# Performance work log

Measured on AMD Instinct MI355X. Metric: run time of the kernel, lower is better.

The kernel has to match this reference:

```python
import jax, jax.numpy as jnp
import numpy as np

EPS = 1e-5  # torch LayerNorm default


def _layer_norm(x, w, b):
    # normalized_shape = [C, K, K] -> normalize over last 3 dims
    m = jnp.mean(x, axis=(-3, -2, -1), keepdims=True)
    v = jnp.var(x, axis=(-3, -2, -1), keepdims=True)
    return (x - m) * jax.lax.rsqrt(v + EPS) * w + b


def setup_inputs() -> dict:
    key = jax.random.key(0)
    k0, k1, k2, k3, k4, k5 = jax.random.split(key, 6)
    B, C, H, W, K = 32, 192, 56, 56, 7
    x = jax.random.normal(k0, (B, C, H, W), jnp.float32)
    ln0_w = jax.random.normal(k1, (C, K, K), jnp.float32)
    ln0_b = jax.random.normal(k2, (C, K, K), jnp.float32)
    conv0_w = jax.random.normal(k3, (C, 1, K, K), jnp.float32) * 0.1
    ln1_w = jax.random.normal(k4, (C, K, K), jnp.float32)
    ln1_b = jax.random.normal(k5, (C, K, K), jnp.float32)
    return {"x": x, "ln0_w": ln0_w, "ln0_b": ln0_b, "conv0_w": conv0_w,
            "ln1_w": ln1_w, "ln1_b": ln1_b}


def reference(x, ln0_w, ln0_b, conv0_w, ln1_w, ln1_b):
    B, C, H, W = x.shape
    K = conv0_w.shape[-1]
    # AdaptiveAvgPool2d((K,K)); H,W divisible by K -> uniform average pooling
    p = x.reshape(B, C, K, H // K, K, W // K).mean(axis=(3, 5))  # [B,C,K,K]
    p = _layer_norm(p, ln0_w, ln0_b)
    # depthwise KxK conv on KxK map, padding 'same'
    p = jax.lax.conv_general_dilated(
        p, conv0_w, window_strides=(1, 1), padding='SAME',
        dimension_numbers=('NCHW', 'OIHW', 'NCHW'), feature_group_count=C)
    p = jax.nn.relu(_layer_norm(p, ln1_w, ln1_b))  # [B,C,K,K] dynamic kernels
    # per-sample, per-channel depthwise conv: fold batch into channels
    ker = p.reshape(B * C, 1, K, K)
    out = jax.lax.conv_general_dilated(
        x.reshape(1, B * C, H, W), ker, window_strides=(1, 1), padding='SAME',
        dimension_numbers=('NCHW', 'OIHW', 'NCHW'), feature_group_count=B * C)
    return out.reshape(B, C, H, W)
```

## Files before the change

### kernel.cpp

```cpp
#include <hip/hip_runtime.h>

#define BB 32
#define CC 192
#define HH 56
#define WW 56
#define KS 7
#define HW 3136
#define KK 49
#define CKK 9408
#define PL 8
#define NCELL (BB * CC * KK)
#define NBC (BB * CC)
#define P0BLK 37
#define MIDBLK 24

typedef float f2 __attribute__((ext_vector_type(2)));

__global__ __launch_bounds__(256) void pool_kernel(const float* __restrict__ x,
                                                   float* __restrict__ p0,
                                                   float2* __restrict__ part0) {
    __shared__ float red[8];
    int b = blockIdx.x / P0BLK;
    int t = blockIdx.x - b * P0BLK;
    int cell = t * 256 + threadIdx.x;
    float v = 0.f;
    if (cell < CKK) {
        int c = cell / KK;
        int r = cell - c * KK;
        int i = r / KS;
        int j = r - i * KS;
        const float* src = x + ((size_t)(b * CC + c)) * HW + (i * PL) * WW + j * PL;
        float s = 0.f;
#pragma unroll
        for (int a = 0; a < PL; ++a) {
            float4 v0 = *(const float4*)(src + a * WW);
            float4 v1 = *(const float4*)(src + a * WW + 4);
            s += v0.x + v0.y + v0.z + v0.w + v1.x + v1.y + v1.z + v1.w;
        }
        v = s * (1.f / 64.f);
        p0[b * CKK + cell] = v;
    }
    float sv = v, sq = v * v;
#pragma unroll
    for (int o = 32; o > 0; o >>= 1) {
        sv += __shfl_down(sv, o, 64);
        sq += __shfl_down(sq, o, 64);
    }
    if ((threadIdx.x & 63) == 0) {
        red[(threadIdx.x >> 6) * 2 + 0] = sv;
        red[(threadIdx.x >> 6) * 2 + 1] = sq;
    }
    __syncthreads();
    if (threadIdx.x == 0)
        part0[blockIdx.x] = make_float2(red[0] + red[2] + red[4] + red[6],
                                        red[1] + red[3] + red[5] + red[7]);
}

__global__ __launch_bounds__(512) void mid_kernel(
    const float* __restrict__ p0,
    const float* __restrict__ ln0w, const float* __restrict__ ln0b,
    const float* __restrict__ w0,
    const float2* __restrict__ part0,
    float* __restrict__ q1,
    float2* __restrict__ part1)
{
    __shared__ float red[16];
    int tid  = threadIdx.x;
    int lane = tid & 63;
    int bc   = blockIdx.x * 8 + (tid >> 6);
    int b = bc / CC;
    int c = bc - b * CC;

    float s0 = 0.f, ss0 = 0.f;
    if (lane < P0BLK) {
        float2 p = part0[b * P0BLK + lane];
        s0 = p.x; ss0 = p.y;
    }
#pragma unroll
    for (int o = 32; o > 0; o >>= 1) {
        s0  += __shfl_down(s0, o, 64);
        ss0 += __shfl_down(ss0, o, 64);
    }
    s0  = __shfl(s0, 0, 64);
    ss0 = __shfl(ss0, 0, 64);
    float mean = s0 * (1.f / CKK);
    float rstd = rsqrtf(ss0 * (1.f / CKK) - mean * mean + 1e-5f);

    float val = 0.f;
    if (lane < KK)
        val = (p0[bc * KK + lane] - mean) * rstd * ln0w[c * KK + lane]
              + ln0b[c * KK + lane];

    int i0 = lane / KS;
    int j0 = lane - i0 * KS;
    const float* wc = w0 + c * KK;

    float acc = 0.f;
#pragma unroll
    for (int u = 0; u < KS; ++u) {
        int ii = i0 + u - 3;
#pragma unroll
        for (int v = 0; v < KS; ++v) {
            int jj = j0 + v - 3;
            bool ok = (ii >= 0) && (ii < KS) && (jj >= 0) && (jj < KS);
            int sl = ok ? (ii * KS + jj) : 0;
            float sv = __shfl(val, sl, 64);
            acc += ok ? sv * wc[u * KS + v] : 0.f;
        }
    }
    if (lane >= KK) acc = 0.f;
    if (lane < KK) q1[bc * KK + lane] = acc;

    float s2 = acc, ss2 = acc * acc;
#pragma unroll
    for (int o = 32; o > 0; o >>= 1) {
        s2  += __shfl_down(s2, o, 64);
        ss2 += __shfl_down(ss2, o, 64);
    }
    if (lane == 0) {
        red[(tid >> 6) * 2 + 0] = s2;
        red[(tid >> 6) * 2 + 1] = ss2;
    }
    __syncthreads();
    if (tid == 0) {
        float a = 0.f, q = 0.f;
#pragma unroll
        for (int w = 0; w < 8; ++w) { a += red[2 * w]; q += red[2 * w + 1]; }
        part1[blockIdx.x] = make_float2(a, q);
    }
}

#define TW2 64

__device__ __forceinline__ float rfl(float v) {
    return __int_as_float(__builtin_amdgcn_readfirstlane(__float_as_int(v)));
}

__device__ __forceinline__ void pkfma_dl(f2& acc, f2 vp, f2 tp) {
    asm("v_pk_fma_f32 %0, %1, %2, %0 op_sel_hi:[1,0,1]"
        : "+v"(acc) : "v"(vp), "s"(tp));
}
__device__ __forceinline__ void pkfma_dh(f2& acc, f2 vp, f2 tp) {
    asm("v_pk_fma_f32 %0, %1, %2, %0 op_sel:[0,1,0] op_sel_hi:[1,1,1]"
        : "+v"(acc) : "v"(vp), "s"(tp));
}
__device__ __forceinline__ void pkfma_x(f2& acc, f2 vp, f2 tp) {
    asm("v_pk_fma_f32 %0, %1, %2, %0 op_sel:[1,0,0] op_sel_hi:[0,1,1]"
        : "+v"(acc) : "v"(vp), "s"(tp));
}

__global__ __launch_bounds__(256) void conv_kernel(
    const float* __restrict__ x,
    const float* __restrict__ q1, const float2* __restrict__ part1,
    const float* __restrict__ ln1w, const float* __restrict__ ln1b,
    float* __restrict__ out)
{
    __shared__ f2 tile2[32 * TW2];
    __shared__ float kt[KK];
    __shared__ f2 dtab[16];
    __shared__ f2 ctab[28];
    int bc   = blockIdx.x;
    int b    = bc / CC;
    int c    = bc - b * CC;
    int tid  = threadIdx.x;
    int lane = tid & 63;
    int wid  = tid >> 6;

    float s1 = 0.f, ss1 = 0.f;
    if (lane < MIDBLK) {
        float2 p = part1[b * MIDBLK + lane];
        s1 = p.x; ss1 = p.y;
    }
#pragma unroll
    for (int o = 32; o > 0; o >>= 1) {
        s1  += __shfl_down(s1, o, 64);
        ss1 += __shfl_down(ss1, o, 64);
    }
    s1  = __shfl(s1, 0, 64);
    ss1 = __shfl(ss1, 0, 64);

    if (tid < KK) {
        float m = s1 * (1.f / CKK);
        float r = rsqrtf(ss1 * (1.f / CKK) - m * m + 1e-5f);
        float v = (q1[(size_t)bc * KK + tid] - m) * r * ln1w[c * KK + tid]
                  + ln1b[c * KK + tid];
        kt[tid] = v > 0.f ? v : 0.f;
    }

    for (int i = tid; i < 32 * TW2 / 2; i += 256)
        ((float4*)tile2)[i] = make_float4(0.f, 0.f, 0.f, 0.f);
    __syncthreads();

    if (tid < 28) {
        int d = tid / KS, v = tid - KS * d;
        f2 p;
        p.x = (d < 3) ? kt[(2 * d + 1) * KS + v] : 0.f;
        p.y = (d > 0) ? kt[(2 * d - 1) * KS + v] : 0.f;
        ctab[tid] = p;
    } else if (tid < 44) {
        int t = tid - 28;
        int d = t / 4, j = t - 4 * d;
        f2 p;
        p.x = kt[2 * d * KS + 2 * j];
        p.y = (2 * j + 1 < KS) ? kt[2 * d * KS + 2 * j + 1] : 0.f;
        dtab[t] = p;
    }

    const float* src = x + (size_t)bc * HW;
    for (int i = tid; i < 29 * 14; i += 256) {
        int pr2 = 1 + i / 14;
        int q   = i - (pr2 - 1) * 14;
        int rA  = 2 * pr2 - 3;
        int rB  = rA + 1;
        float4 a4 = (rA >= 0) ? *(const float4*)(src + rA * WW + 4 * q)
                              : make_float4(0.f, 0.f, 0.f, 0.f);
        float4 b4 = (rB < HH) ? *(const float4*)(src + rB * WW + 4 * q)
                              : make_float4(0.f, 0.f, 0.f, 0.f);
        f2* cell = tile2 + pr2 * TW2 + 3 + 4 * q;
        cell[0] = (f2){a4.x, b4.x};
        cell[1] = (f2){a4.y, b4.y};
        cell[2] = (f2){a4.z, b4.z};
        cell[3] = (f2){a4.w, b4.w};
    }
    __syncthreads();

    f2 dp[16], cp[28];
#pragma unroll
    for (int i = 0; i < 8; ++i) {
        float4 t4 = ((const float4*)dtab)[i];
        dp[2 * i]     = (f2){rfl(t4.x), rfl(t4.y)};
        dp[2 * i + 1] = (f2){rfl(t4.z), rfl(t4.w)};
    }
#pragma unroll
    for (int i = 0; i < 14; ++i) {
        float4 t4 = ((const float4*)ctab)[i];
        cp[2 * i]     = (f2){rfl(t4.x), rfl(t4.y)};
        cp[2 * i + 1] = (f2){rfl(t4.z), rfl(t4.w)};
    }

    int r0 = wid * 14;
    int R2 = wid * 7;
    f2 acc2[7];
#pragma unroll
    for (int t = 0; t < 7; ++t) acc2[t] = (f2){0.f, 0.f};

#pragma unroll
    for (int s = 0; s < 10; ++s) {
        const f2* cellp = tile2 + (R2 + s) * TW2 + lane;
        f2 v2[KS];
#pragma unroll
        for (int j = 0; j < KS; ++j) v2[j] = cellp[j];
#pragma unroll
        for (int d = 0; d < 4; ++d) {
            int t = s - d;
            if (t < 0 || t > 6) continue;
#pragma unroll
            for (int v = 0; v < KS; ++v) {
                if (v & 1) pkfma_dh(acc2[t], v2[v], dp[d * 4 + (v >> 1)]);
                else       pkfma_dl(acc2[t], v2[v], dp[d * 4 + (v >> 1)]);
                pkfma_x(acc2[t], v2[v], cp[d * KS + v]);
            }
        }
    }

    if (lane < WW) {
        float* ob = out + (size_t)bc * HW + r0 * WW + lane;
#pragma unroll
        for (int t = 0; t < 7; ++t) {
            ob[(2 * t) * WW]     = acc2[t].x;
            ob[(2 * t + 1) * WW] = acc2[t].y;
        }
    }
}

extern "C" void kernel_launch(void* const* d_in, const int* in_sizes, int n_in,
                              void* d_out, int out_size, void* d_ws, size_t ws_size,
                              hipStream_t stream) {
    const float* x    = (const float*)d_in[0];
    const float* ln0w = (const float*)d_in[1];
    const float* ln0b = (const float*)d_in[2];
    const float* w0   = (const float*)d_in[3];
    const float* ln1w = (const float*)d_in[4];
    const float* ln1b = (const float*)d_in[5];
    float* out = (float*)d_out;

    float*  p0    = (float*)d_ws;
    float*  q1    = p0 + NCELL;
    float2* part0 = (float2*)(q1 + NCELL);
    float2* part1 = part0 + BB * P0BLK;

    pool_kernel<<<BB * P0BLK, 256, 0, stream>>>(x, p0, part0);
    mid_kernel <<<BB * MIDBLK, 512, 0, stream>>>(p0, ln0w, ln0b, w0, part0, q1, part1);
    conv_kernel<<<NBC, 256, 0, stream>>>(x, q1, part1, ln1w, ln1b, out);
}
```

Measured before the change: 67.56 us.

## Compute two adjacent output columns per thread in conv kernel with 128 threads

The depthwise conv kernel drops from 256 to 128 threads per block. Each lane now computes two neighbouring output columns across 14 rows, sharing eight loaded input values, and reads LDS as float4 and writes output as float2. This halves the wavefront count and cuts LDS loads per FMA. The cost is more accumulator registers per thread and less thread-level parallelism per block.

Result: slower. 71.70 us (+6.1%).

```diff
diff --git a/kernel.cpp b/kernel.cpp
--- a/kernel.cpp
+++ b/kernel.cpp
@@ -149,7 +149,7 @@
         : "+v"(acc) : "v"(vp), "s"(tp));
 }
 
-__global__ __launch_bounds__(256) void conv_kernel(
+__global__ __launch_bounds__(128) void conv_kernel(
     const float* __restrict__ x,
     const float* __restrict__ q1, const float2* __restrict__ part1,
     const float* __restrict__ ln1w, const float* __restrict__ ln1b,
@@ -187,7 +187,7 @@
         kt[tid] = v > 0.f ? v : 0.f;
     }
 
-    for (int i = tid; i < 32 * TW2 / 2; i += 256)
+    for (int i = tid; i < 32 * TW2 / 2; i += 128)
         ((float4*)tile2)[i] = make_float4(0.f, 0.f, 0.f, 0.f);
     __syncthreads();
 
@@ -207,7 +207,7 @@
     }
 
     const float* src = x + (size_t)bc * HW;
-    for (int i = tid; i < 29 * 14; i += 256) {
+    for (int i = tid; i < 29 * 14; i += 128) {
         int pr2 = 1 + i / 14;
         int q   = i - (pr2 - 1) * 14;
         int rA  = 2 * pr2 - 3;
@@ -224,7 +224,7 @@
     }
     __syncthreads();
 
-    f2 dp[16], cp[28];
+    f2 dp[16], cpx[28];
 #pragma unroll
     for (int i = 0; i < 8; ++i) {
         float4 t4 = ((const float4*)dtab)[i];
@@ -234,41 +234,57 @@
 #pragma unroll
     for (int i = 0; i < 14; ++i) {
         float4 t4 = ((const float4*)ctab)[i];
-        cp[2 * i]     = (f2){rfl(t4.x), rfl(t4.y)};
-        cp[2 * i + 1] = (f2){rfl(t4.z), rfl(t4.w)};
-    }
-
-    int r0 = wid * 14;
-    int R2 = wid * 7;
-    f2 acc2[7];
-#pragma unroll
-    for (int t = 0; t < 7; ++t) acc2[t] = (f2){0.f, 0.f};
+        cpx[2 * i]     = (f2){rfl(t4.x), rfl(t4.y)};
+        cpx[2 * i + 1] = (f2){rfl(t4.z), rfl(t4.w)};
+    }
+
+    int rh = lane / 28;  if (rh > 1) rh = 1;
+    int cp = lane - 28 * (lane / 28); if (cp > 27) cp = 27;
+    int R2 = wid * 14 + rh * 7;
+
+    f2 accA[7], accB[7];
+#pragma unroll
+    for (int t = 0; t < 7; ++t) { accA[t] = (f2){0.f, 0.f}; accB[t] = (f2){0.f, 0.f}; }
 
 #pragma unroll
     for (int s = 0; s < 10; ++s) {
-        const f2* cellp = tile2 + (R2 + s) * TW2 + lane;
-        f2 v2[KS];
-#pragma unroll
-        for (int j = 0; j < KS; ++j) v2[j] = cellp[j];
+        const float4* rp = (const float4*)(tile2 + (R2 + s) * TW2 + 2 * cp);
+        float4 q0 = rp[0], q1v = rp[1], q2 = rp[2], q3 = rp[3];
+        f2 v2[8];
+        v2[0] = (f2){q0.x, q0.y}; v2[1] = (f2){q0.z, q0.w};
+        v2[2] = (f2){q1v.x, q1v.y}; v2[3] = (f2){q1v.z, q1v.w};
+        v2[4] = (f2){q2.x, q2.y}; v2[5] = (f2){q2.z, q2.w};
+        v2[6] = (f2){q3.x, q3.y}; v2[7] = (f2){q3.z, q3.w};
 #pragma unroll
         for (int d = 0; d < 4; ++d) {
             int t = s - d;
             if (t < 0 || t > 6) continue;
 #pragma unroll
-            for (int v = 0; v < KS; ++v) {
-                if (v & 1) pkfma_dh(acc2[t], v2[v], dp[d * 4 + (v >> 1)]);
-                else       pkfma_dl(acc2[t], v2[v], dp[d * 4 + (v >> 1)]);
-                pkfma_x(acc2[t], v2[v], cp[d * KS + v]);
+            for (int j = 0; j < 7; ++j) {
+                if (j & 1) pkfma_dh(accA[t], v2[j], dp[d * 4 + (j >> 1)]);
+                else       pkfma_dl(accA[t], v2[j], dp[d * 4 + (j >> 1)]);
+                pkfma_x(accA[t], v2[j], cpx[d * KS + j]);
+            }
+#pragma unroll
+            for (int j = 1; j < 8; ++j) {
+                int v = j - 1;
+                if (v & 1) pkfma_dh(accB[t], v2[j], dp[d * 4 + (v >> 1)]);
+                else       pkfma_dl(accB[t], v2[j], dp[d * 4 + (v >> 1)]);
+                pkfma_x(accB[t], v2[j], cpx[d * KS + v]);
             }
         }
     }
 
-    if (lane < WW) {
-        float* ob = out + (size_t)bc * HW + r0 * WW + lane;
+    if (lane < 56) {
+        float* ob = out + (size_t)bc * HW;
+        int col = 2 * cp;
+        int rowbase = wid * 28 + rh * 14;
 #pragma unroll
         for (int t = 0; t < 7; ++t) {
-            ob[(2 * t) * WW]     = acc2[t].x;
-            ob[(2 * t + 1) * WW] = acc2[t].y;
+            *(float2*)(ob + (rowbase + 2 * t) * WW + col) =
+                make_float2(accA[t].x, accB[t].x);
+            *(float2*)(ob + (rowbase + 2 * t + 1) * WW + col) =
+                make_float2(accA[t].y, accB[t].y);
         }
     }
 }
@@ -291,5 +307,5 @@
 
     pool_kernel<<<BB * P0BLK, 256, 0, stream>>>(x, p0, part0);
     mid_kernel <<<BB * MIDBLK, 512, 0, stream>>>(p0, ln0w, ln0b, w0, part0, q1, part1);
-    conv_kernel<<<NBC, 256, 0, stream>>>(x, q1, part1, ln1w, ln1b, out);
-}
+    conv_kernel<<<NBC, 128, 0, stream>>>(x, q1, part1, ln1w, ln1b, out);
+}
```

## Precompute dynamic kernel tables in separate kernel and prefetch input before barrier

Applied to the files above, without the earlier changes.

Moves the LayerNorm1/ReLU and packed coefficient-table construction out of the conv kernel into a new tab_kernel, one wave per (b,c), built with shuffles instead of shared memory. The conv kernel then loads the 44 packed coefficients straight from global memory. It also issues the input row loads into registers before the tile-zeroing barrier, so the load latency overlaps the zeroing. This removes a barrier and the per-block LN work from the conv kernel, at the cost of an extra kernel launch and a small workspace round trip. The coefficients are now loaded as uniform values without readfirstlane, so the compiler may have to prove uniformity to keep them in SGPRs.

Result: slower. 69.54 us (+2.9%).

```diff
diff --git a/kernel.cpp b/kernel.cpp
--- a/kernel.cpp
+++ b/kernel.cpp
@@ -130,41 +130,15 @@
     }
 }
 
-#define TW2 64
-
-__device__ __forceinline__ float rfl(float v) {
-    return __int_as_float(__builtin_amdgcn_readfirstlane(__float_as_int(v)));
-}
-
-__device__ __forceinline__ void pkfma_dl(f2& acc, f2 vp, f2 tp) {
-    asm("v_pk_fma_f32 %0, %1, %2, %0 op_sel_hi:[1,0,1]"
-        : "+v"(acc) : "v"(vp), "s"(tp));
-}
-__device__ __forceinline__ void pkfma_dh(f2& acc, f2 vp, f2 tp) {
-    asm("v_pk_fma_f32 %0, %1, %2, %0 op_sel:[0,1,0] op_sel_hi:[1,1,1]"
-        : "+v"(acc) : "v"(vp), "s"(tp));
-}
-__device__ __forceinline__ void pkfma_x(f2& acc, f2 vp, f2 tp) {
-    asm("v_pk_fma_f32 %0, %1, %2, %0 op_sel:[1,0,0] op_sel_hi:[0,1,1]"
-        : "+v"(acc) : "v"(vp), "s"(tp));
-}
-
-__global__ __launch_bounds__(256) void conv_kernel(
-    const float* __restrict__ x,
+__global__ __launch_bounds__(256) void tab_kernel(
     const float* __restrict__ q1, const float2* __restrict__ part1,
     const float* __restrict__ ln1w, const float* __restrict__ ln1b,
-    float* __restrict__ out)
+    f2* __restrict__ tab)
 {
-    __shared__ f2 tile2[32 * TW2];
-    __shared__ float kt[KK];
-    __shared__ f2 dtab[16];
-    __shared__ f2 ctab[28];
-    int bc   = blockIdx.x;
-    int b    = bc / CC;
-    int c    = bc - b * CC;
-    int tid  = threadIdx.x;
-    int lane = tid & 63;
-    int wid  = tid >> 6;
+    int lane = threadIdx.x & 63;
+    int bc   = blockIdx.x * 4 + (threadIdx.x >> 6);
+    int b = bc / CC;
+    int c = bc - b * CC;
 
     float s1 = 0.f, ss1 = 0.f;
     if (lane < MIDBLK) {
@@ -178,65 +152,114 @@
     }
     s1  = __shfl(s1, 0, 64);
     ss1 = __shfl(ss1, 0, 64);
-
-    if (tid < KK) {
-        float m = s1 * (1.f / CKK);
-        float r = rsqrtf(ss1 * (1.f / CKK) - m * m + 1e-5f);
-        float v = (q1[(size_t)bc * KK + tid] - m) * r * ln1w[c * KK + tid]
-                  + ln1b[c * KK + tid];
-        kt[tid] = v > 0.f ? v : 0.f;
+    float m = s1 * (1.f / CKK);
+    float r = rsqrtf(ss1 * (1.f / CKK) - m * m + 1e-5f);
+
+    float kt = 0.f;
+    if (lane < KK) {
+        float v = (q1[(size_t)bc * KK + lane] - m) * r * ln1w[c * KK + lane]
+                  + ln1b[c * KK + lane];
+        kt = v > 0.f ? v : 0.f;
+    }
+
+    int iA = 0, iB = 0;
+    bool mA = false, mB = false;
+    if (lane < 28) {
+        int d = lane / KS, v = lane - KS * d;
+        mA = (d < 3); iA = mA ? (2 * d + 1) * KS + v : 0;
+        mB = (d > 0); iB = mB ? (2 * d - 1) * KS + v : 0;
+    } else if (lane < 44) {
+        int t = lane - 28;
+        int d = t >> 2, j = t & 3;
+        mA = true;     iA = 2 * d * KS + 2 * j;
+        mB = (j < 3);  iB = mB ? 2 * d * KS + 2 * j + 1 : 0;
+    }
+    float va = __shfl(kt, iA, 64);
+    float vb = __shfl(kt, iB, 64);
+    f2 p;
+    p.x = mA ? va : 0.f;
+    p.y = mB ? vb : 0.f;
+
+    f2* row = tab + (size_t)bc * 44;
+    if (lane < 28)      row[16 + lane] = p;
+    else if (lane < 44) row[lane - 28] = p;
+}
+
+#define TW2 64
+
+__device__ __forceinline__ void pkfma_dl(f2& acc, f2 vp, f2 tp) {
+    asm("v_pk_fma_f32 %0, %1, %2, %0 op_sel_hi:[1,0,1]"
+        : "+v"(acc) : "v"(vp), "s"(tp));
+}
+__device__ __forceinline__ void pkfma_dh(f2& acc, f2 vp, f2 tp) {
+    asm("v_pk_fma_f32 %0, %1, %2, %0 op_sel:[0,1,0] op_sel_hi:[1,1,1]"
+        : "+v"(acc) : "v"(vp), "s"(tp));
+}
+__device__ __forceinline__ void pkfma_x(f2& acc, f2 vp, f2 tp) {
+    asm("v_pk_fma_f32 %0, %1, %2, %0 op_sel:[1,0,0] op_sel_hi:[0,1,1]"
+        : "+v"(acc) : "v"(vp), "s"(tp));
+}
+
+__global__ __launch_bounds__(256) void conv_kernel(
+    const float* __restrict__ x,
+    const f2* __restrict__ tab,
+    float* __restrict__ out)
+{
+    __shared__ f2 tile2[32 * TW2];
+    int bc   = blockIdx.x;
+    int tid  = threadIdx.x;
+    int lane = tid & 63;
+    int wid  = tid >> 6;
+
+    const float4* tb4 = (const float4*)(tab + (size_t)bc * 44);
+    f2 dp[16], cpx[28];
+#pragma unroll
+    for (int i = 0; i < 8; ++i) {
+        float4 t4 = tb4[i];
+        dp[2 * i]     = (f2){t4.x, t4.y};
+        dp[2 * i + 1] = (f2){t4.z, t4.w};
+    }
+#pragma unroll
+    for (int i = 0; i < 14; ++i) {
+        float4 t4 = tb4[8 + i];
+        cpx[2 * i]     = (f2){t4.x, t4.y};
+        cpx[2 * i + 1] = (f2){t4.z, t4.w};
+    }
+
+    const float* src = x + (size_t)bc * HW;
+    int t0 = tid, t1 = tid + 256;
+    int pr2a = 1 + t0 / 14, qa = t0 - (pr2a - 1) * 14;
+    int pr2b = 1 + t1 / 14, qb = t1 - (pr2b - 1) * 14;
+    int rAa = 2 * pr2a - 3, rBa = rAa + 1;
+    int rAb = 2 * pr2b - 3, rBb = rAb + 1;
+    float4 z4 = make_float4(0.f, 0.f, 0.f, 0.f);
+    float4 a0 = (rAa >= 0) ? *(const float4*)(src + rAa * WW + 4 * qa) : z4;
+    float4 b0 = (rBa < HH) ? *(const float4*)(src + rBa * WW + 4 * qa) : z4;
+    float4 a1 = z4, b1 = z4;
+    if (t1 < 29 * 14) {
+        a1 = *(const float4*)(src + rAb * WW + 4 * qb);
+        b1 = (rBb < HH) ? *(const float4*)(src + rBb * WW + 4 * qb) : z4;
     }
 
     for (int i = tid; i < 32 * TW2 / 2; i += 256)
-        ((float4*)tile2)[i] = make_float4(0.f, 0.f, 0.f, 0.f);
+        ((float4*)tile2)[i] = z4;
     __syncthreads();
 
-    if (tid < 28) {
-        int d = tid / KS, v = tid - KS * d;
-        f2 p;
-        p.x = (d < 3) ? kt[(2 * d + 1) * KS + v] : 0.f;
-        p.y = (d > 0) ? kt[(2 * d - 1) * KS + v] : 0.f;
-        ctab[tid] = p;
-    } else if (tid < 44) {
-        int t = tid - 28;
-        int d = t / 4, j = t - 4 * d;
-        f2 p;
-        p.x = kt[2 * d * KS + 2 * j];
-        p.y = (2 * j + 1 < KS) ? kt[2 * d * KS + 2 * j + 1] : 0.f;
-        dtab[t] = p;
-    }
-
-    const float* src = x + (size_t)bc * HW;
-    for (int i = tid; i < 29 * 14; i += 256) {
-        int pr2 = 1 + i / 14;
-        int q   = i - (pr2 - 1) * 14;
-        int rA  = 2 * pr2 - 3;
-        int rB  = rA + 1;
-        float4 a4 = (rA >= 0) ? *(const float4*)(src + rA * WW + 4 * q)
-                              : make_float4(0.f, 0.f, 0.f, 0.f);
-        float4 b4 = (rB < HH) ? *(const float4*)(src + rB * WW + 4 * q)
-                              : make_float4(0.f, 0.f, 0.f, 0.f);
-        f2* cell = tile2 + pr2 * TW2 + 3 + 4 * q;
-        cell[0] = (f2){a4.x, b4.x};
-        cell[1] = (f2){a4.y, b4.y};
-        cell[2] = (f2){a4.z, b4.z};
-        cell[3] = (f2){a4.w, b4.w};
+    {
+        f2* cell = tile2 + pr2a * TW2 + 3 + 4 * qa;
+        cell[0] = (f2){a0.x, b0.x};
+        cell[1] = (f2){a0.y, b0.y};
+        cell[2] = (f2){a0.z, b0.z};
+        cell[3] = (f2){a0.w, b0.w};
+    }
+    if (t1 < 29 * 14) {
+        f2* cell = tile2 + pr2b * TW2 + 3 + 4 * qb;
+        cell[0] = (f2){a1.x, b1.x};
+        cell[1] = (f2){a1.y, b1.y};
+        cell[2] = (f2){a1.z, b1.z};
+        cell[3] = (f2){a1.w, b1.w};
     }
     __syncthreads();
-
-    f2 dp[16], cp[28];
-#pragma unroll
-    for (int i = 0; i < 8; ++i) {
-        float4 t4 = ((const float4*)dtab)[i];
-        dp[2 * i]     = (f2){rfl(t4.x), rfl(t4.y)};
-        dp[2 * i + 1] = (f2){rfl(t4.z), rfl(t4.w)};
-    }
-#pragma unroll
-    for (int i = 0; i < 14; ++i) {
-        float4 t4 = ((const float4*)ctab)[i];
-        cp[2 * i]     = (f2){rfl(t4.x), rfl(t4.y)};
-        cp[2 * i + 1] = (f2){rfl(t4.z), rfl(t4.w)};
-    }
 
     int r0 = wid * 14;
     int R2 = wid * 7;
@@ -258,7 +281,7 @@
             for (int v = 0; v < KS; ++v) {
                 if (v & 1) pkfma_dh(acc2[t], v2[v], dp[d * 4 + (v >> 1)]);
                 else       pkfma_dl(acc2[t], v2[v], dp[d * 4 + (v >> 1)]);
-                pkfma_x(acc2[t], v2[v], cp[d * KS + v]);
+                pkfma_x(acc2[t], v2[v], cpx[d * KS + v]);
             }
         }
     }
@@ -288,8 +311,10 @@
     float*  q1    = p0 + NCELL;
     float2* part0 = (float2*)(q1 + NCELL);
     float2* part1 = part0 + BB * P0BLK;
+    f2*     tab   = (f2*)(part1 + BB * MIDBLK);
 
     pool_kernel<<<BB * P0BLK, 256, 0, stream>>>(x, p0, part0);
     mid_kernel <<<BB * MIDBLK, 512, 0, stream>>>(p0, ln0w, ln0b, w0, part0, q1, part1);
-    conv_kernel<<<NBC, 256, 0, stream>>>(x, q1, part1, ln1w, ln1b, out);
-}
+    tab_kernel <<<NBC / 4, 256, 0, stream>>>(q1, part1, ln1w, ln1b, tab);
+    conv_kernel<<<NBC, 256, 0, stream>>>(x, tab, out);
+}
```

## Split dynamic-kernel LayerNorm into separate kernel and use per-wave LDS tiles with scalar FMAs

Applied to the files above, without the earlier changes.

Moves the second LayerNorm+ReLU that builds each dynamic 7x7 kernel out of the conv kernel into a new tab_kernel, which writes the taps to a workspace table. The conv kernel then loads the taps as wave-uniform scalars and drops block-wide __syncthreads by giving each wave its own LDS strip of interleaved row pairs. It also replaces the inline-asm packed FMAs with plain scalar fmaf. This removes per-block prologue and synchronisation cost, but adds an extra launch and roughly doubles the FMA instruction count in the inner loop.

After: 75.83 us. 12.2% more time.

```diff
diff --git a/kernel.cpp b/kernel.cpp
--- a/kernel.cpp
+++ b/kernel.cpp
@@ -13,6 +13,7 @@
 #define NBC (BB * CC)
 #define P0BLK 37
 #define MIDBLK 24
+#define KSTRIDE 52
 
 typedef float f2 __attribute__((ext_vector_type(2)));
 
@@ -130,41 +131,15 @@
     }
 }
 
-#define TW2 64
-
-__device__ __forceinline__ float rfl(float v) {
-    return __int_as_float(__builtin_amdgcn_readfirstlane(__float_as_int(v)));
-}
-
-__device__ __forceinline__ void pkfma_dl(f2& acc, f2 vp, f2 tp) {
-    asm("v_pk_fma_f32 %0, %1, %2, %0 op_sel_hi:[1,0,1]"
-        : "+v"(acc) : "v"(vp), "s"(tp));
-}
-__device__ __forceinline__ void pkfma_dh(f2& acc, f2 vp, f2 tp) {
-    asm("v_pk_fma_f32 %0, %1, %2, %0 op_sel:[0,1,0] op_sel_hi:[1,1,1]"
-        : "+v"(acc) : "v"(vp), "s"(tp));
-}
-__device__ __forceinline__ void pkfma_x(f2& acc, f2 vp, f2 tp) {
-    asm("v_pk_fma_f32 %0, %1, %2, %0 op_sel:[1,0,0] op_sel_hi:[0,1,1]"
-        : "+v"(acc) : "v"(vp), "s"(tp));
-}
-
-__global__ __launch_bounds__(256) void conv_kernel(
-    const float* __restrict__ x,
+__global__ __launch_bounds__(256) void tab_kernel(
     const float* __restrict__ q1, const float2* __restrict__ part1,
     const float* __restrict__ ln1w, const float* __restrict__ ln1b,
-    float* __restrict__ out)
+    float* __restrict__ ktab)
 {
-    __shared__ f2 tile2[32 * TW2];
-    __shared__ float kt[KK];
-    __shared__ f2 dtab[16];
-    __shared__ f2 ctab[28];
-    int bc   = blockIdx.x;
-    int b    = bc / CC;
-    int c    = bc - b * CC;
-    int tid  = threadIdx.x;
-    int lane = tid & 63;
-    int wid  = tid >> 6;
+    int lane = threadIdx.x & 63;
+    int bc   = blockIdx.x * 4 + (threadIdx.x >> 6);
+    int b = bc / CC;
+    int c = bc - b * CC;
 
     float s1 = 0.f, ss1 = 0.f;
     if (lane < MIDBLK) {
@@ -178,87 +153,75 @@
     }
     s1  = __shfl(s1, 0, 64);
     ss1 = __shfl(ss1, 0, 64);
-
-    if (tid < KK) {
-        float m = s1 * (1.f / CKK);
-        float r = rsqrtf(ss1 * (1.f / CKK) - m * m + 1e-5f);
-        float v = (q1[(size_t)bc * KK + tid] - m) * r * ln1w[c * KK + tid]
-                  + ln1b[c * KK + tid];
-        kt[tid] = v > 0.f ? v : 0.f;
-    }
-
-    for (int i = tid; i < 32 * TW2 / 2; i += 256)
-        ((float4*)tile2)[i] = make_float4(0.f, 0.f, 0.f, 0.f);
-    __syncthreads();
-
-    if (tid < 28) {
-        int d = tid / KS, v = tid - KS * d;
-        f2 p;
-        p.x = (d < 3) ? kt[(2 * d + 1) * KS + v] : 0.f;
-        p.y = (d > 0) ? kt[(2 * d - 1) * KS + v] : 0.f;
-        ctab[tid] = p;
-    } else if (tid < 44) {
-        int t = tid - 28;
-        int d = t / 4, j = t - 4 * d;
-        f2 p;
-        p.x = kt[2 * d * KS + 2 * j];
-        p.y = (2 * j + 1 < KS) ? kt[2 * d * KS + 2 * j + 1] : 0.f;
-        dtab[t] = p;
-    }
+    float m = s1 * (1.f / CKK);
+    float r = rsqrtf(ss1 * (1.f / CKK) - m * m + 1e-5f);
+
+    if (lane < KK) {
+        float v = (q1[(size_t)bc * KK + lane] - m) * r * ln1w[c * KK + lane]
+                  + ln1b[c * KK + lane];
+        ktab[(size_t)bc * KSTRIDE + lane] = v > 0.f ? v : 0.f;
+    }
+}
+
+__device__ __forceinline__ float rfl(float v) {
+    return __int_as_float(__builtin_amdgcn_readfirstlane(__float_as_int(v)));
+}
+
+__global__ __launch_bounds__(256) void conv_kernel(
+    const float* __restrict__ x,
+    const float* __restrict__ ktab,
+    float* __restrict__ out)
+{
+    __shared__ f2 wl[4][10 * 64];
+    int bc   = blockIdx.x;
+    int tid  = threadIdx.x;
+    int lane = tid & 63;
+    int wid  = tid >> 6;
+
+    const float* kp = ktab + (size_t)bc * KSTRIDE;
+    float tap[KK];
+#pragma unroll
+    for (int t = 0; t < KK; ++t) tap[t] = rfl(kp[t]);
 
     const float* src = x + (size_t)bc * HW;
-    for (int i = tid; i < 29 * 14; i += 256) {
-        int pr2 = 1 + i / 14;
-        int q   = i - (pr2 - 1) * 14;
-        int rA  = 2 * pr2 - 3;
-        int rB  = rA + 1;
-        float4 a4 = (rA >= 0) ? *(const float4*)(src + rA * WW + 4 * q)
-                              : make_float4(0.f, 0.f, 0.f, 0.f);
-        float4 b4 = (rB < HH) ? *(const float4*)(src + rB * WW + 4 * q)
-                              : make_float4(0.f, 0.f, 0.f, 0.f);
-        f2* cell = tile2 + pr2 * TW2 + 3 + 4 * q;
-        cell[0] = (f2){a4.x, b4.x};
-        cell[1] = (f2){a4.y, b4.y};
-        cell[2] = (f2){a4.z, b4.z};
-        cell[3] = (f2){a4.w, b4.w};
-    }
-    __syncthreads();
-
-    f2 dp[16], cp[28];
-#pragma unroll
-    for (int i = 0; i < 8; ++i) {
-        float4 t4 = ((const float4*)dtab)[i];
-        dp[2 * i]     = (f2){rfl(t4.x), rfl(t4.y)};
-        dp[2 * i + 1] = (f2){rfl(t4.z), rfl(t4.w)};
-    }
-#pragma unroll
-    for (int i = 0; i < 14; ++i) {
-        float4 t4 = ((const float4*)ctab)[i];
-        cp[2 * i]     = (f2){rfl(t4.x), rfl(t4.y)};
-        cp[2 * i + 1] = (f2){rfl(t4.z), rfl(t4.w)};
-    }
-
-    int r0 = wid * 14;
-    int R2 = wid * 7;
-    f2 acc2[7];
-#pragma unroll
-    for (int t = 0; t < 7; ++t) acc2[t] = (f2){0.f, 0.f};
+    int r0   = wid * 14;
+    int colx = lane - 3;
+    bool colok = (colx >= 0) && (colx < WW);
+    f2* wlp = wl[wid];
+#pragma unroll
+    for (int k = 0; k < 10; ++k) {
+        int rlo = r0 - 3 + 2 * k;
+        int rhi = rlo + 1;
+        float vlo = 0.f, vhi = 0.f;
+        if (colok && rlo >= 0 && rlo < HH) vlo = src[rlo * WW + colx];
+        if (colok && rhi >= 0 && rhi < HH) vhi = src[rhi * WW + colx];
+        wlp[k * 64 + lane] = (f2){vlo, vhi};
+    }
+    asm volatile("s_waitcnt lgkmcnt(0)" ::: "memory");
+    __builtin_amdgcn_sched_barrier(0);
+
+    float accL[7], accH[7];
+#pragma unroll
+    for (int t = 0; t < 7; ++t) { accL[t] = 0.f; accH[t] = 0.f; }
 
 #pragma unroll
     for (int s = 0; s < 10; ++s) {
-        const f2* cellp = tile2 + (R2 + s) * TW2 + lane;
-        f2 v2[KS];
-#pragma unroll
-        for (int j = 0; j < KS; ++j) v2[j] = cellp[j];
+        const f2* cp = wlp + s * 64 + lane;
+        f2 v[KS];
+#pragma unroll
+        for (int j = 0; j < KS; ++j) v[j] = cp[j];
 #pragma unroll
         for (int d = 0; d < 4; ++d) {
             int t = s - d;
             if (t < 0 || t > 6) continue;
 #pragma unroll
-            for (int v = 0; v < KS; ++v) {
-                if (v & 1) pkfma_dh(acc2[t], v2[v], dp[d * 4 + (v >> 1)]);
-                else       pkfma_dl(acc2[t], v2[v], dp[d * 4 + (v >> 1)]);
-                pkfma_x(acc2[t], v2[v], cp[d * KS + v]);
+            for (int vv = 0; vv < KS; ++vv) {
+                accL[t] = fmaf(v[vv].x, tap[2 * d * KS + vv], accL[t]);
+                if (2 * d + 1 <= 6)
+                    accL[t] = fmaf(v[vv].y, tap[(2 * d + 1) * KS + vv], accL[t]);
+                if (2 * d - 1 >= 0)
+                    accH[t] = fmaf(v[vv].x, tap[(2 * d - 1) * KS + vv], accH[t]);
+                accH[t] = fmaf(v[vv].y, tap[2 * d * KS + vv], accH[t]);
             }
         }
     }
@@ -267,8 +230,8 @@
         float* ob = out + (size_t)bc * HW + r0 * WW + lane;
 #pragma unroll
         for (int t = 0; t < 7; ++t) {
-            ob[(2 * t) * WW]     = acc2[t].x;
-            ob[(2 * t + 1) * WW] = acc2[t].y;
+            ob[(2 * t) * WW]     = accL[t];
+            ob[(2 * t + 1) * WW] = accH[t];
         }
     }
 }
@@ -288,8 +251,10 @@
     float*  q1    = p0 + NCELL;
     float2* part0 = (float2*)(q1 + NCELL);
     float2* part1 = part0 + BB * P0BLK;
+    float*  ktab  = (float*)(part1 + BB * MIDBLK);
 
     pool_kernel<<<BB * P0BLK, 256, 0, stream>>>(x, p0, part0);
     mid_kernel <<<BB * MIDBLK, 512, 0, stream>>>(p0, ln0w, ln0b, w0, part0, q1, part1);
-    conv_kernel<<<NBC, 256, 0, stream>>>(x, q1, part1, ln1w, ln1b, out);
-}
+    tab_kernel <<<NBC / 4, 256, 0, stream>>>(q1, part1, ln1w, ln1b, ktab);
+    conv_kernel<<<NBC, 256, 0, stream>>>(x, ktab, out);
+}
```
